# Kernel tuning notes

Measured on AMD Instinct MI355X. Metric: run time of the kernel, lower is better.

Reference implementation:

```python
import jax, jax.numpy as jnp
import numpy as np

NEG_SLOPE = 0.2

def gat_conv(x, src, dst, n, W, a_src, a_dst, b):
    # PyG GATConv, heads=1: h = xW; e_ij = LeakyReLU(a_src.h_j + a_dst.h_i)
    # alpha = softmax over incoming edges of i; out_i = sum_j alpha_ij * h_j + b
    h = x @ W                               # [N, F_out]
    s_src = h @ a_src                       # [N]
    s_dst = h @ a_dst                       # [N]
    e = s_src[src] + s_dst[dst]             # [E]
    e = jnp.where(e > 0, e, NEG_SLOPE * e)  # leaky relu
    # numerically stable scatter-softmax over destination groups
    m = jax.ops.segment_max(e, dst, num_segments=n)          # [N]
    ee = jnp.exp(e - m[dst])                                  # [E]
    denom = jax.ops.segment_sum(ee, dst, num_segments=n)      # [N]
    alpha = ee / denom[dst]                                    # [E]
    out = jax.ops.segment_sum(alpha[:, None] * h[src], dst, num_segments=n)
    return out + b

def add_self_loops(edge_index, n):
    loops = jnp.arange(n, dtype=edge_index.dtype)
    src = jnp.concatenate([edge_index[0], loops])
    dst = jnp.concatenate([edge_index[1], loops])
    return src, dst

def setup_inputs() -> dict:
    key = jax.random.key(0)
    ks = jax.random.split(key, 12)
    N, E, F_IN, H1, H2, C = 50000, 800000, 1433, 512, 256, 7
    x = jax.random.normal(ks[0], (N, F_IN), dtype=jnp.float32)
    edge_index = jax.random.randint(ks[1], (2, E), 0, N, dtype=jnp.int64)
    def glorot(k, shape):
        lim = float(np.sqrt(6.0 / (shape[0] + shape[-1])))
        return jax.random.uniform(k, shape, jnp.float32, -lim, lim)
    params = {
        'W1': glorot(ks[2], (F_IN, H1)), 'as1': glorot(ks[3], (H1,)), 'ad1': glorot(ks[4], (H1,)), 'b1': jnp.zeros((H1,), jnp.float32),
        'W2': glorot(ks[5], (H1, H2)), 'as2': glorot(ks[6], (H2,)), 'ad2': glorot(ks[7], (H2,)), 'b2': jnp.zeros((H2,), jnp.float32),
        'W3': glorot(ks[8], (H2, C)), 'as3': glorot(ks[9], (C,)), 'ad3': glorot(ks[10], (C,)), 'b3': jnp.zeros((C,), jnp.float32),
    }
    return {'x': x, 'edge_index': edge_index, **params}

def reference(x, edge_index, W1, as1, ad1, b1, W2, as2, ad2, b2, W3, as3, ad3, b3):
    n = x.shape[0]
    src, dst = add_self_loops(edge_index, n)
    h = jax.nn.relu(gat_conv(x, src, dst, n, W1, as1, ad1, b1))
    h = jax.nn.relu(gat_conv(h, src, dst, n, W2, as2, ad2, b2))
    h = gat_conv(h, src, dst, n, W3, as3, ad3, b3)
    return jax.nn.log_softmax(h, axis=1)
```

## Files before the change

kernel.cpp:

```cpp
#include <hip/hip_runtime.h>
#include <math.h>

constexpr int N_NODES = 50000;
constexpr int E_EDGES = 800000;
constexpr int E_TOT   = E_EDGES + N_NODES;
constexpr int F_IN  = 1433;
constexpr int KPAD1 = 1440;
constexpr int F1 = 512;
constexpr int F2 = 256;
constexpr int NC = 7;
constexpr int MAXDEG = 1024;
constexpr float NEG_SLOPE = 0.2f;

typedef unsigned short u16;
typedef unsigned int   u32;
typedef short s16x8 __attribute__((ext_vector_type(8)));
typedef float f32x4 __attribute__((ext_vector_type(4)));

__device__ inline u16 f2b(float f) {
    u32 u = __float_as_uint(f);
    u32 r = (u + 0x7fffu + ((u >> 16) & 1u)) >> 16;
    return (u16)r;
}
__device__ inline float b2f(u16 b) { return __uint_as_float(((u32)b) << 16); }

__device__ inline void gload_lds16(const void* g, void* l) {
    __builtin_amdgcn_global_load_lds(
        (const __attribute__((address_space(1))) u32*)g,
        (__attribute__((address_space(3))) u32*)l, 16, 0, 0);
}

__global__ void count_dst_kernel(const int* __restrict__ dst, int* __restrict__ counts) {
    int i = blockIdx.x * blockDim.x + threadIdx.x;
    if (i < E_TOT) {
        int d = (i < E_EDGES) ? dst[i] : (i - E_EDGES);
        atomicAdd(&counts[d], 1);
    }
}

__global__ __launch_bounds__(1024) void scan_kernel(const int* __restrict__ counts,
                                                    int* __restrict__ row_ptr, int n) {
    __shared__ int part[1024];
    int t = threadIdx.x;
    int chunk = (n + 1023) / 1024;
    int lo = t * chunk;
    int hi = min(lo + chunk, n);
    int s = 0;
    for (int i = lo; i < hi; ++i) s += counts[i];
    part[t] = s;
    __syncthreads();
    for (int off = 1; off < 1024; off <<= 1) {
        int v = 0;
        if (t >= off) v = part[t - off];
        __syncthreads();
        part[t] += v;
        __syncthreads();
    }
    int run = part[t] - s;
    for (int i = lo; i < hi; ++i) { row_ptr[i] = run; run += counts[i]; }
    if (t == 1023) row_ptr[n] = part[1023];
}

__global__ void scatter_kernel(const int* __restrict__ src, const int* __restrict__ dst,
                               const int* __restrict__ row_ptr, int* __restrict__ fill,
                               int* __restrict__ col) {
    int i = blockIdx.x * blockDim.x + threadIdx.x;
    if (i < E_TOT) {
        int s = (i < E_EDGES) ? src[i] : (i - E_EDGES);
        int d = (i < E_EDGES) ? dst[i] : (i - E_EDGES);
        int p = row_ptr[d] + atomicAdd(&fill[d], 1);
        col[p] = s;
    }
}

__global__ void convert_x_kernel(const float* __restrict__ x, u32* __restrict__ xb) {
    constexpr int PPR = KPAD1 / 2;
    int p = blockIdx.x * blockDim.x + threadIdx.x;
    if (p >= N_NODES * PPR) return;
    int row = p / PPR;
    int c = (p - row * PPR) * 2;
    const float* xr = x + (size_t)row * F_IN;
    float v0 = (c + 0 < F_IN) ? xr[c + 0] : 0.f;
    float v1 = (c + 1 < F_IN) ? xr[c + 1] : 0.f;
    xb[p] = (u32)f2b(v0) | ((u32)f2b(v1) << 16);
}

__global__ void convert_wt_kernel(const float* __restrict__ W, u32* __restrict__ Wt,
                                  int K, int Nn, int KP) {
    int p = blockIdx.x * blockDim.x + threadIdx.x;
    int ppr = KP / 2;
    if (p >= Nn * ppr) return;
    int n = p / ppr;
    int k = (p - n * ppr) * 2;
    float v0 = (k + 0 < K) ? W[(size_t)(k + 0) * Nn + n] : 0.f;
    float v1 = (k + 1 < K) ? W[(size_t)(k + 1) * Nn + n] : 0.f;
    Wt[p] = (u32)f2b(v0) | ((u32)f2b(v1) << 16);
}

__global__ __launch_bounds__(256) void mfma_gemm_bt(const u16* __restrict__ A,
                                                    const u16* __restrict__ Bt,
                                                    u16* __restrict__ C,
                                                    int M, int N, int K) {
    __shared__ u16 sA[128 * 32];
    __shared__ u16 sB[128 * 32];
    int tid  = threadIdx.x;
    int wave = tid >> 6;
    int lane = tid & 63;
    int quad = lane >> 4;
    int lm   = lane & 15;
    int wm = wave & 1;
    int wn = wave >> 1;
    int m0 = blockIdx.y * 128;
    int n0 = blockIdx.x * 128;

    int ch0 = wave * 2, ch1 = wave * 2 + 1;
    int rsub = lane >> 2;
    int csub = (lane & 3) * 8;
    int ar0 = min(m0 + ch0 * 16 + rsub, M - 1);
    int ar1 = min(m0 + ch1 * 16 + rsub, M - 1);
    int br0 = n0 + ch0 * 16 + rsub;
    int br1 = n0 + ch1 * 16 + rsub;
    const u16* gA0 = A + (size_t)ar0 * K + csub;
    const u16* gA1 = A + (size_t)ar1 * K + csub;
    const u16* gB0 = Bt + (size_t)br0 * K + csub;
    const u16* gB1 = Bt + (size_t)br1 * K + csub;

    f32x4 acc[4][4];
#pragma unroll
    for (int i = 0; i < 4; ++i)
#pragma unroll
        for (int j = 0; j < 4; ++j) acc[i][j] = (f32x4){0.f, 0.f, 0.f, 0.f};

    for (int k0 = 0; k0 < K; k0 += 32) {
        gload_lds16(gA0 + k0, &sA[ch0 * 512]);
        gload_lds16(gA1 + k0, &sA[ch1 * 512]);
        gload_lds16(gB0 + k0, &sB[ch0 * 512]);
        gload_lds16(gB1 + k0, &sB[ch1 * 512]);
        __syncthreads();

        s16x8 af[4], bf[4];
#pragma unroll
        for (int mt = 0; mt < 4; ++mt)
            af[mt] = *(const s16x8*)&sA[(wm * 64 + mt * 16 + lm) * 32 + quad * 8];
#pragma unroll
        for (int nt = 0; nt < 4; ++nt)
            bf[nt] = *(const s16x8*)&sB[(wn * 64 + nt * 16 + lm) * 32 + quad * 8];
#pragma unroll
        for (int mt = 0; mt < 4; ++mt)
#pragma unroll
            for (int nt = 0; nt < 4; ++nt)
                acc[mt][nt] = __builtin_amdgcn_mfma_f32_16x16x32_bf16(
                    af[mt], bf[nt], acc[mt][nt], 0, 0, 0);
        __syncthreads();
    }

#pragma unroll
    for (int mt = 0; mt < 4; ++mt) {
        int mbase = m0 + wm * 64 + mt * 16 + quad * 4;
#pragma unroll
        for (int nt = 0; nt < 4; ++nt) {
            int n = n0 + wn * 64 + nt * 16 + lm;
#pragma unroll
            for (int r = 0; r < 4; ++r) {
                int m = mbase + r;
                if (m < M) C[(size_t)m * N + n] = f2b(acc[mt][nt][r]);
            }
        }
    }
}

template <int F>
__global__ __launch_bounds__(256) void scores_bf16_kernel(const u16* __restrict__ h,
                                                          const float* __restrict__ a_src,
                                                          const float* __restrict__ a_dst,
                                                          float* __restrict__ s_src,
                                                          float* __restrict__ s_dst, int n) {
    int gwid = (blockIdx.x * blockDim.x + threadIdx.x) >> 6;
    int lane = threadIdx.x & 63;
    if (gwid >= n) return;
    const u32* row = (const u32*)(h + (size_t)gwid * F);
    float acc1 = 0.f, acc2 = 0.f;
    for (int p = lane; p < F / 2; p += 64) {
        u32 u = row[p];
        float v0 = b2f((u16)(u & 0xffff));
        float v1 = b2f((u16)(u >> 16));
        acc1 += v0 * a_src[2 * p] + v1 * a_src[2 * p + 1];
        acc2 += v0 * a_dst[2 * p] + v1 * a_dst[2 * p + 1];
    }
#pragma unroll
    for (int o = 32; o; o >>= 1) {
        acc1 += __shfl_xor(acc1, o);
        acc2 += __shfl_xor(acc2, o);
    }
    if (lane == 0) { s_src[gwid] = acc1; s_dst[gwid] = acc2; }
}

template <int F>
__global__ __launch_bounds__(256) void scores_kernel(const float* __restrict__ h,
                                                     const float* __restrict__ a_src,
                                                     const float* __restrict__ a_dst,
                                                     float* __restrict__ s_src,
                                                     float* __restrict__ s_dst, int n) {
    int gwid = (blockIdx.x * blockDim.x + threadIdx.x) >> 6;
    int lane = threadIdx.x & 63;
    if (gwid >= n) return;
    const float* row = h + (size_t)gwid * F;
    float acc1 = 0.f, acc2 = 0.f;
    for (int f = lane; f < F; f += 64) {
        float v = row[f];
        acc1 += v * a_src[f];
        acc2 += v * a_dst[f];
    }
#pragma unroll
    for (int o = 32; o; o >>= 1) {
        acc1 += __shfl_xor(acc1, o);
        acc2 += __shfl_xor(acc2, o);
    }
    if (lane == 0) { s_src[gwid] = acc1; s_dst[gwid] = acc2; }
}

template <int F, bool OUT_BF16>
__global__ __launch_bounds__(F / 2) void agg_bf16_kernel(const u16* __restrict__ h,
                                                         const float* __restrict__ s_src,
                                                         const float* __restrict__ s_dst,
                                                         const float* __restrict__ bias,
                                                         const int* __restrict__ row_ptr,
                                                         const int* __restrict__ col,
                                                         void* __restrict__ out) {
    constexpr int TPB = F / 2;
    int node = blockIdx.x;
    int tid = threadIdx.x;
    int beg = row_ptr[node];
    int deg = min(row_ptr[node + 1] - beg, MAXDEG);

    __shared__ float w[MAXDEG];
    __shared__ int cs[MAXDEG];
    __shared__ float sdenom;

    if (tid < 64) {
        float sd = s_dst[node];
        float m = -1e30f;
        for (int j = tid; j < deg; j += 64) {
            int s = col[beg + j];
            cs[j] = s;
            float e = s_src[s] + sd;
            e = (e > 0.f) ? e : NEG_SLOPE * e;
            w[j] = e;
            m = fmaxf(m, e);
        }
#pragma unroll
        for (int o = 32; o; o >>= 1) m = fmaxf(m, __shfl_xor(m, o));
        float sum = 0.f;
        for (int j = tid; j < deg; j += 64) {
            float v = expf(w[j] - m);
            w[j] = v;
            sum += v;
        }
#pragma unroll
        for (int o = 32; o; o >>= 1) sum += __shfl_xor(sum, o);
        if (tid == 0) sdenom = sum;
    }
    __syncthreads();
    float inv = 1.0f / sdenom;

    float a0 = 0.f, a1 = 0.f;
    for (int j = 0; j < deg; ++j) {
        float wg = w[j] * inv;
        u32 u = ((const u32*)(h + (size_t)cs[j] * F))[tid];
        a0 += wg * b2f((u16)(u & 0xffff));
        a1 += wg * b2f((u16)(u >> 16));
    }
    float v0 = fmaxf(a0 + bias[2 * tid], 0.f);
    float v1 = fmaxf(a1 + bias[2 * tid + 1], 0.f);
    if (OUT_BF16) {
        ((u32*)out)[(size_t)node * TPB + tid] = (u32)f2b(v0) | ((u32)f2b(v1) << 16);
    } else {
        ((float2*)out)[(size_t)node * TPB + tid] = make_float2(v0, v1);
    }
}

template <int F, int TPB>
__global__ __launch_bounds__(TPB) void aggregate_lsm_kernel(const float* __restrict__ h,
                                                            const float* __restrict__ s_src,
                                                            const float* __restrict__ s_dst,
                                                            const float* __restrict__ bias,
                                                            const int* __restrict__ row_ptr,
                                                            const int* __restrict__ col,
                                                            float* __restrict__ out) {
    int node = blockIdx.x;
    int tid = threadIdx.x;
    int beg = row_ptr[node];
    int deg = min(row_ptr[node + 1] - beg, MAXDEG);

    __shared__ float w[MAXDEG];
    __shared__ int cs[MAXDEG];
    __shared__ float sdenom;

    if (tid < 64) {
        float sd = s_dst[node];
        float m = -1e30f;
        for (int j = tid; j < deg; j += 64) {
            int s = col[beg + j];
            cs[j] = s;
            float e = s_src[s] + sd;
            e = (e > 0.f) ? e : NEG_SLOPE * e;
            w[j] = e;
            m = fmaxf(m, e);
        }
#pragma unroll
        for (int o = 32; o; o >>= 1) m = fmaxf(m, __shfl_xor(m, o));
        float sum = 0.f;
        for (int j = tid; j < deg; j += 64) {
            float v = expf(w[j] - m);
            w[j] = v;
            sum += v;
        }
#pragma unroll
        for (int o = 32; o; o >>= 1) sum += __shfl_xor(sum, o);
        if (tid == 0) sdenom = sum;
    }
    __syncthreads();
    float inv = 1.0f / sdenom;

    float acc = 0.f;
    for (int j = 0; j < deg; ++j) {
        float wg = w[j] * inv;
        if (tid < F) acc += wg * h[(size_t)cs[j] * F + tid];
    }

    __shared__ float vals[F];
    if (tid < F) vals[tid] = acc + bias[tid];
    __syncthreads();
    if (tid < F) {
        float mx = -1e30f;
#pragma unroll
        for (int i = 0; i < F; ++i) mx = fmaxf(mx, vals[i]);
        float ssum = 0.f;
#pragma unroll
        for (int i = 0; i < F; ++i) ssum += expf(vals[i] - mx);
        out[(size_t)node * F + tid] = vals[tid] - mx - logf(ssum);
    }
}

__global__ __launch_bounds__(256) void gemm3_kernel(const float* __restrict__ A,
                                                    const float* __restrict__ W,
                                                    float* __restrict__ out, int n) {
    __shared__ float sW[F2 * NC];
    for (int i = threadIdx.x; i < F2 * NC; i += blockDim.x) sW[i] = W[i];
    __syncthreads();
    int gwid = (blockIdx.x * blockDim.x + threadIdx.x) >> 6;
    int lane = threadIdx.x & 63;
    if (gwid >= n) return;
    const float* row = A + (size_t)gwid * F2;
    float4 v = *(const float4*)(row + lane * 4);
    float res = 0.f;
#pragma unroll
    for (int c = 0; c < NC; ++c) {
        float p = v.x * sW[(lane * 4 + 0) * NC + c] + v.y * sW[(lane * 4 + 1) * NC + c] +
                  v.z * sW[(lane * 4 + 2) * NC + c] + v.w * sW[(lane * 4 + 3) * NC + c];
#pragma unroll
        for (int o = 32; o; o >>= 1) p += __shfl_xor(p, o);
        if (lane == c) res = p;
    }
    if (lane < NC) out[(size_t)gwid * NC + lane] = res;
}

extern "C" void kernel_launch(void* const* d_in, const int* in_sizes, int n_in,
                              void* d_out, int out_size, void* d_ws, size_t ws_size,
                              hipStream_t stream) {
    const float* x   = (const float*)d_in[0];
    const int* ei    = (const int*)d_in[1];
    const int* src   = ei;
    const int* dst   = ei + E_EDGES;
    const float* W1  = (const float*)d_in[2];
    const float* as1 = (const float*)d_in[3];
    const float* ad1 = (const float*)d_in[4];
    const float* b1  = (const float*)d_in[5];
    const float* W2  = (const float*)d_in[6];
    const float* as2 = (const float*)d_in[7];
    const float* ad2 = (const float*)d_in[8];
    const float* b2  = (const float*)d_in[9];
    const float* W3  = (const float*)d_in[10];
    const float* as3 = (const float*)d_in[11];
    const float* ad3 = (const float*)d_in[12];
    const float* b3  = (const float*)d_in[13];
    float* outp = (float*)d_out;

    char* base = (char*)d_ws;
    u16*  xb  = (u16*)base;
    u16*  a1b = (u16*)base;
    u16*  h2b = (u16*)(base + 51200000);
    float* a2 = (float*)(base + 76800000);
    float* h3 = (float*)(base + 128000000);
    u16*  h1b = (u16*)(base + 144000000);
    u16*  W1t = (u16*)(base + 195200000);
    u16*  W2t = (u16*)(base + 196674560);
    float* ssrc = (float*)(base + 196936704);
    float* sdst = (float*)(base + 197136704);
    int* row_ptr = (int*)(base + 197336704);
    int* counts  = (int*)(base + 197536708);
    int* fill    = (int*)(base + 197736708);
    int* col     = (int*)(base + 197936708);

    hipMemsetAsync(counts, 0, sizeof(int) * N_NODES, stream);
    hipMemsetAsync(fill, 0, sizeof(int) * N_NODES, stream);

    {
        int blk = 256;
        int grid = (E_TOT + blk - 1) / blk;
        count_dst_kernel<<<grid, blk, 0, stream>>>(dst, counts);
        scan_kernel<<<1, 1024, 0, stream>>>(counts, row_ptr, N_NODES);
        scatter_kernel<<<grid, blk, 0, stream>>>(src, dst, row_ptr, fill, col);
    }

    {
        int np = N_NODES * (KPAD1 / 2);
        convert_x_kernel<<<(np + 255) / 256, 256, 0, stream>>>(x, (u32*)xb);
        int nw1 = F1 * (KPAD1 / 2);
        convert_wt_kernel<<<(nw1 + 255) / 256, 256, 0, stream>>>(W1, (u32*)W1t, F_IN, F1, KPAD1);
        int nw2 = F2 * (F1 / 2);
        convert_wt_kernel<<<(nw2 + 255) / 256, 256, 0, stream>>>(W2, (u32*)W2t, F1, F2, F1);
    }

    int waves_grid = (N_NODES + 3) / 4;
    int mblocks = (N_NODES + 127) / 128;

    {
        dim3 grid(F1 / 128, mblocks);
        mfma_gemm_bt<<<grid, 256, 0, stream>>>(xb, W1t, h1b, N_NODES, F1, KPAD1);
        scores_bf16_kernel<F1><<<waves_grid, 256, 0, stream>>>(h1b, as1, ad1, ssrc, sdst, N_NODES);
        agg_bf16_kernel<F1, true><<<N_NODES, F1 / 2, 0, stream>>>(
            h1b, ssrc, sdst, b1, row_ptr, col, a1b);
    }
    {
        dim3 grid(F2 / 128, mblocks);
        mfma_gemm_bt<<<grid, 256, 0, stream>>>(a1b, W2t, h2b, N_NODES, F2, F1);
        scores_bf16_kernel<F2><<<waves_grid, 256, 0, stream>>>(h2b, as2, ad2, ssrc, sdst, N_NODES);
        agg_bf16_kernel<F2, false><<<N_NODES, F2 / 2, 0, stream>>>(
            h2b, ssrc, sdst, b2, row_ptr, col, a2);
    }
    {
        gemm3_kernel<<<waves_grid, 256, 0, stream>>>(a2, W3, h3, N_NODES);
        scores_kernel<NC><<<waves_grid, 256, 0, stream>>>(h3, as3, ad3, ssrc, sdst, N_NODES);
        aggregate_lsm_kernel<NC, 64><<<N_NODES, 64, 0, stream>>>(
            h3, ssrc, sdst, b3, row_ptr, col, outp);
    }
}
```

Before: 1.127 ms.

## Split neighbor gather across four waves with vector loads and shared-memory reduction

The bf16 aggregation kernels now use 256 threads per node. Four waves each take a strided subset of the incoming edges, two edges per iteration, and each lane loads 8 or 16 bytes of a neighbor row. Partial sums are combined through a shared-memory reduction before the bias, ReLU and store. The final 7-class aggregation is rewritten so one wave spreads the edges across lanes and reduces with shuffles, instead of idling 57 of its 64 threads. This aims to add memory-level parallelism to the latency-bound gather, at the cost of extra shared memory and a second barrier per node.

```diff
diff --git a/kernel.cpp b/kernel.cpp
--- a/kernel.cpp
+++ b/kernel.cpp
@@ -220,27 +220,30 @@
 }
 
 template <int F, bool OUT_BF16>
-__global__ __launch_bounds__(F / 2) void agg_bf16_kernel(const u16* __restrict__ h,
+__global__ __launch_bounds__(256) void agg_gather_kernel(const u16* __restrict__ h,
                                                          const float* __restrict__ s_src,
                                                          const float* __restrict__ s_dst,
                                                          const float* __restrict__ bias,
                                                          const int* __restrict__ row_ptr,
                                                          const int* __restrict__ col,
                                                          void* __restrict__ out) {
-    constexpr int TPB = F / 2;
+    constexpr int UPL = F / 128;
     int node = blockIdx.x;
     int tid = threadIdx.x;
+    int wave = tid >> 6;
+    int lane = tid & 63;
     int beg = row_ptr[node];
     int deg = min(row_ptr[node + 1] - beg, MAXDEG);
 
     __shared__ float w[MAXDEG];
     __shared__ int cs[MAXDEG];
     __shared__ float sdenom;
-
-    if (tid < 64) {
+    __shared__ float red[4][F];
+
+    if (wave == 0) {
         float sd = s_dst[node];
         float m = -1e30f;
-        for (int j = tid; j < deg; j += 64) {
+        for (int j = lane; j < deg; j += 64) {
             int s = col[beg + j];
             cs[j] = s;
             float e = s_src[s] + sd;
@@ -251,94 +254,141 @@
 #pragma unroll
         for (int o = 32; o; o >>= 1) m = fmaxf(m, __shfl_xor(m, o));
         float sum = 0.f;
-        for (int j = tid; j < deg; j += 64) {
+        for (int j = lane; j < deg; j += 64) {
             float v = expf(w[j] - m);
             w[j] = v;
             sum += v;
         }
 #pragma unroll
         for (int o = 32; o; o >>= 1) sum += __shfl_xor(sum, o);
-        if (tid == 0) sdenom = sum;
+        if (lane == 0) sdenom = sum;
     }
     __syncthreads();
     float inv = 1.0f / sdenom;
 
-    float a0 = 0.f, a1 = 0.f;
-    for (int j = 0; j < deg; ++j) {
+    float acc[2 * UPL];
+#pragma unroll
+    for (int e = 0; e < 2 * UPL; ++e) acc[e] = 0.f;
+
+    int j = wave;
+    for (; j + 4 < deg; j += 8) {
+        float wg0 = w[j] * inv;
+        float wg1 = w[j + 4] * inv;
+        const u32* r0 = (const u32*)(h + (size_t)cs[j] * F) + lane * UPL;
+        const u32* r1 = (const u32*)(h + (size_t)cs[j + 4] * F) + lane * UPL;
+        u32 v0[UPL], v1[UPL];
+        if constexpr (UPL == 4) {
+            uint4 q0 = *(const uint4*)r0; v0[0] = q0.x; v0[1] = q0.y; v0[2] = q0.z; v0[3] = q0.w;
+            uint4 q1 = *(const uint4*)r1; v1[0] = q1.x; v1[1] = q1.y; v1[2] = q1.z; v1[3] = q1.w;
+        } else {
+            uint2 q0 = *(const uint2*)r0; v0[0] = q0.x; v0[1] = q0.y;
+            uint2 q1 = *(const uint2*)r1; v1[0] = q1.x; v1[1] = q1.y;
+        }
+#pragma unroll
+        for (int u = 0; u < UPL; ++u) {
+            acc[2 * u]     += wg0 * b2f((u16)(v0[u] & 0xffff)) + wg1 * b2f((u16)(v1[u] & 0xffff));
+            acc[2 * u + 1] += wg0 * b2f((u16)(v0[u] >> 16))    + wg1 * b2f((u16)(v1[u] >> 16));
+        }
+    }
+    if (j < deg) {
         float wg = w[j] * inv;
-        u32 u = ((const u32*)(h + (size_t)cs[j] * F))[tid];
-        a0 += wg * b2f((u16)(u & 0xffff));
-        a1 += wg * b2f((u16)(u >> 16));
-    }
-    float v0 = fmaxf(a0 + bias[2 * tid], 0.f);
-    float v1 = fmaxf(a1 + bias[2 * tid + 1], 0.f);
-    if (OUT_BF16) {
-        ((u32*)out)[(size_t)node * TPB + tid] = (u32)f2b(v0) | ((u32)f2b(v1) << 16);
+        const u32* r = (const u32*)(h + (size_t)cs[j] * F) + lane * UPL;
+        u32 v[UPL];
+        if constexpr (UPL == 4) {
+            uint4 q = *(const uint4*)r; v[0] = q.x; v[1] = q.y; v[2] = q.z; v[3] = q.w;
+        } else {
+            uint2 q = *(const uint2*)r; v[0] = q.x; v[1] = q.y;
+        }
+#pragma unroll
+        for (int u = 0; u < UPL; ++u) {
+            acc[2 * u]     += wg * b2f((u16)(v[u] & 0xffff));
+            acc[2 * u + 1] += wg * b2f((u16)(v[u] >> 16));
+        }
+    }
+
+#pragma unroll
+    for (int e = 0; e < 2 * UPL; ++e) red[wave][lane * 2 * UPL + e] = acc[e];
+    __syncthreads();
+
+    if constexpr (OUT_BF16) {
+        if (tid < F / 2) {
+            int f = tid * 2;
+            float v0 = red[0][f] + red[1][f] + red[2][f] + red[3][f] + bias[f];
+            float v1 = red[0][f + 1] + red[1][f + 1] + red[2][f + 1] + red[3][f + 1] + bias[f + 1];
+            v0 = fmaxf(v0, 0.f);
+            v1 = fmaxf(v1, 0.f);
+            ((u32*)out)[(size_t)node * (F / 2) + tid] = (u32)f2b(v0) | ((u32)f2b(v1) << 16);
+        }
     } else {
-        ((float2*)out)[(size_t)node * TPB + tid] = make_float2(v0, v1);
-    }
-}
-
-template <int F, int TPB>
-__global__ __launch_bounds__(TPB) void aggregate_lsm_kernel(const float* __restrict__ h,
-                                                            const float* __restrict__ s_src,
-                                                            const float* __restrict__ s_dst,
-                                                            const float* __restrict__ bias,
-                                                            const int* __restrict__ row_ptr,
-                                                            const int* __restrict__ col,
-                                                            float* __restrict__ out) {
+        if (tid < F) {
+            float v = red[0][tid] + red[1][tid] + red[2][tid] + red[3][tid] + bias[tid];
+            ((float*)out)[(size_t)node * F + tid] = fmaxf(v, 0.f);
+        }
+    }
+}
+
+__global__ __launch_bounds__(64) void agg_lsm7_kernel(const float* __restrict__ h,
+                                                      const float* __restrict__ s_src,
+                                                      const float* __restrict__ s_dst,
+                                                      const float* __restrict__ bias,
+                                                      const int* __restrict__ row_ptr,
+                                                      const int* __restrict__ col,
+                                                      float* __restrict__ out) {
     int node = blockIdx.x;
-    int tid = threadIdx.x;
+    int lane = threadIdx.x;
     int beg = row_ptr[node];
     int deg = min(row_ptr[node + 1] - beg, MAXDEG);
 
     __shared__ float w[MAXDEG];
     __shared__ int cs[MAXDEG];
-    __shared__ float sdenom;
-
-    if (tid < 64) {
-        float sd = s_dst[node];
-        float m = -1e30f;
-        for (int j = tid; j < deg; j += 64) {
-            int s = col[beg + j];
-            cs[j] = s;
-            float e = s_src[s] + sd;
-            e = (e > 0.f) ? e : NEG_SLOPE * e;
-            w[j] = e;
-            m = fmaxf(m, e);
-        }
-#pragma unroll
-        for (int o = 32; o; o >>= 1) m = fmaxf(m, __shfl_xor(m, o));
-        float sum = 0.f;
-        for (int j = tid; j < deg; j += 64) {
-            float v = expf(w[j] - m);
-            w[j] = v;
-            sum += v;
-        }
-#pragma unroll
-        for (int o = 32; o; o >>= 1) sum += __shfl_xor(sum, o);
-        if (tid == 0) sdenom = sum;
-    }
-    __syncthreads();
-    float inv = 1.0f / sdenom;
-
-    float acc = 0.f;
-    for (int j = 0; j < deg; ++j) {
+
+    float sd = s_dst[node];
+    float m = -1e30f;
+    for (int j = lane; j < deg; j += 64) {
+        int s = col[beg + j];
+        cs[j] = s;
+        float e = s_src[s] + sd;
+        e = (e > 0.f) ? e : NEG_SLOPE * e;
+        w[j] = e;
+        m = fmaxf(m, e);
+    }
+#pragma unroll
+    for (int o = 32; o; o >>= 1) m = fmaxf(m, __shfl_xor(m, o));
+    float sum = 0.f;
+    for (int j = lane; j < deg; j += 64) {
+        float v = expf(w[j] - m);
+        w[j] = v;
+        sum += v;
+    }
+#pragma unroll
+    for (int o = 32; o; o >>= 1) sum += __shfl_xor(sum, o);
+    float inv = 1.0f / sum;
+
+    float a[NC];
+#pragma unroll
+    for (int f = 0; f < NC; ++f) a[f] = 0.f;
+    for (int j = lane; j < deg; j += 64) {
         float wg = w[j] * inv;
-        if (tid < F) acc += wg * h[(size_t)cs[j] * F + tid];
-    }
-
-    __shared__ float vals[F];
-    if (tid < F) vals[tid] = acc + bias[tid];
-    __syncthreads();
-    if (tid < F) {
+        const float* row = h + (size_t)cs[j] * NC;
+#pragma unroll
+        for (int f = 0; f < NC; ++f) a[f] += wg * row[f];
+    }
+#pragma unroll
+    for (int f = 0; f < NC; ++f)
+#pragma unroll
+        for (int o = 32; o; o >>= 1) a[f] += __shfl_xor(a[f], o);
+
+    if (lane == 0) {
+        float vals[NC];
         float mx = -1e30f;
 #pragma unroll
-        for (int i = 0; i < F; ++i) mx = fmaxf(mx, vals[i]);
+        for (int f = 0; f < NC; ++f) { vals[f] = a[f] + bias[f]; mx = fmaxf(mx, vals[f]); }
         float ssum = 0.f;
 #pragma unroll
-        for (int i = 0; i < F; ++i) ssum += expf(vals[i] - mx);
-        out[(size_t)node * F + tid] = vals[tid] - mx - logf(ssum);
+        for (int f = 0; f < NC; ++f) ssum += expf(vals[f] - mx);
+        float lse = mx + logf(ssum);
+#pragma unroll
+        for (int f = 0; f < NC; ++f) out[(size_t)node * NC + f] = vals[f] - lse;
     }
 }
 
@@ -429,20 +479,20 @@
         dim3 grid(F1 / 128, mblocks);
         mfma_gemm_bt<<<grid, 256, 0, stream>>>(xb, W1t, h1b, N_NODES, F1, KPAD1);
         scores_bf16_kernel<F1><<<waves_grid, 256, 0, stream>>>(h1b, as1, ad1, ssrc, sdst, N_NODES);
-        agg_bf16_kernel<F1, true><<<N_NODES, F1 / 2, 0, stream>>>(
+        agg_gather_kernel<F1, true><<<N_NODES, 256, 0, stream>>>(
             h1b, ssrc, sdst, b1, row_ptr, col, a1b);
     }
     {
         dim3 grid(F2 / 128, mblocks);
         mfma_gemm_bt<<<grid, 256, 0, stream>>>(a1b, W2t, h2b, N_NODES, F2, F1);
         scores_bf16_kernel<F2><<<waves_grid, 256, 0, stream>>>(h2b, as2, ad2, ssrc, sdst, N_NODES);
-        agg_bf16_kernel<F2, false><<<N_NODES, F2 / 2, 0, stream>>>(
+        agg_gather_kernel<F2, false><<<N_NODES, 256, 0, stream>>>(
             h2b, ssrc, sdst, b2, row_ptr, col, a2);
     }
     {
         gemm3_kernel<<<waves_grid, 256, 0, stream>>>(a2, W3, h3, N_NODES);
         scores_kernel<NC><<<waves_grid, 256, 0, stream>>>(h3, as3, ad3, ssrc, sdst, N_NODES);
-        aggregate_lsm_kernel<NC, 64><<<N_NODES, 64, 0, stream>>>(
+        agg_lsm7_kernel<<<N_NODES, 64, 0, stream>>>(
             h3, ssrc, sdst, b3, row_ptr, col, outp);
     }
 }
```

After: 1.126 ms. Within noise of the previous version (-0.0%).
